# Performance work log

Measured on AMD Instinct MI355X. Metric: run time of the kernel, lower is better.

## Reference

```python
import jax, jax.numpy as jnp
import numpy as np

B, T, C, H = 8, 2048, 512, 512


def setup_inputs() -> dict:
    key = jax.random.key(0)
    ks = jax.random.split(key, 9)
    s = 1.0 / np.sqrt(C)
    return {
        "q": jax.random.normal(ks[0], (B, T, C), jnp.float32),
        "k": jax.random.normal(ks[1], (B, T, C), jnp.float32),
        "v": jax.random.normal(ks[2], (B, T, C), jnp.float32),
        "Wq": jax.random.normal(ks[3], (C, H), jnp.float32) * s,
        "bq": jax.random.normal(ks[4], (H,), jnp.float32) * 0.01,
        "Wk": jax.random.normal(ks[5], (C, H), jnp.float32) * s,
        "bk": jax.random.normal(ks[6], (H,), jnp.float32) * 0.01,
        "Wv": jax.random.normal(ks[7], (C, H), jnp.float32) * s,
        "bv": jax.random.normal(ks[8], (H,), jnp.float32) * 0.01,
    }


def reference(q, k, v, Wq, bq, Wk, bk, Wv, bv):
    # Linear projections (Real_Linear == nn.Linear): [B,T,C] @ [C,H] + [H]
    query = jnp.einsum('btc,ch->bth', q, Wq) + bq
    key_p = jnp.einsum('btc,ch->bth', k, Wk) + bk
    value = jnp.einsum('btc,ch->bth', v, Wv) + bv
    # energy = Q @ K^T / sqrt(H)  -> [B, T, T]
    energy = jnp.einsum('bth,byh->bty', query, key_p) / jnp.sqrt(jnp.asarray(H, query.dtype))
    attn = jax.nn.softmax(energy, axis=-1)
    # weighted value: [B, T, T] @ [B, T, H] -> [B, T, H]
    return jnp.einsum('bty,byh->bth', attn, value)
```

## Files before the change

kernel.cpp:

```cpp
#include <hip/hip_runtime.h>
#include <hip/hip_bf16.h>

typedef unsigned short u16;
typedef unsigned int u32;
typedef short s16x8 __attribute__((ext_vector_type(8)));
typedef float f32x4 __attribute__((ext_vector_type(4)));

#define NB 8
#define NT 2048
#define NC 512
#define NH 512

__device__ __forceinline__ u16 f2bf(float f) {
  unsigned u = __float_as_uint(f);
  u += 0x7FFFu + ((u >> 16) & 1u);
  return (u16)(u >> 16);
}

__device__ __forceinline__ void gld16(const u16* src, u16* lds_dst) {
  __builtin_amdgcn_global_load_lds(
      (const __attribute__((address_space(1))) u32*)src,
      (__attribute__((address_space(3))) u32*)lds_dst, 16, 0, 0);
}

__global__ __launch_bounds__(256) void wt_kernel(const float* __restrict__ W,
                                                 u16* __restrict__ WT) {
  __shared__ float tile[32][33];
  const int x = threadIdx.x & 31;
  const int y = threadIdx.x >> 5;
  const int k0 = blockIdx.x * 32, h0 = blockIdx.y * 32;
#pragma unroll
  for (int p = 0; p < 4; ++p)
    tile[y + 8 * p][x] = W[(size_t)(k0 + y + 8 * p) * NH + h0 + x];
  __syncthreads();
#pragma unroll
  for (int p = 0; p < 4; ++p)
    WT[(size_t)(h0 + y + 8 * p) * NC + k0 + x] = f2bf(tile[x][y + 8 * p]);
}

__global__ __launch_bounds__(256) void proj_kernel(const float* __restrict__ X,
                                                   const u16* __restrict__ WT,
                                                   const float* __restrict__ bias,
                                                   u16* __restrict__ Y) {
  __shared__ __align__(16) u16 Asub[2][128 * 40];
  __shared__ __align__(16) u16 Bsub[2][128 * 40];
  const int t = threadIdx.x;
  const int lane = t & 63;
  const int w = t >> 6;
  const int l16 = lane & 15;
  const int ko8 = (lane >> 4) * 8;
  const int m0 = blockIdx.y * 128;
  const int n0 = blockIdx.x * 128;
  const int wr = (w >> 1) * 64, wc = (w & 1) * 64;
  f32x4 acc[4][4] = {};

  float4 areg[4];
  int4 breg[2];
#define PLOAD(kt)                                                              \
  {                                                                            \
    const int k0_ = (kt) * 32;                                                 \
    _Pragma("unroll")                                                          \
    for (int p = 0; p < 4; ++p) {                                              \
      int c = t + 256 * p;                                                     \
      areg[p] = *(const float4*)&X[(size_t)(m0 + (c >> 3)) * NC + k0_ + (c & 7) * 4]; \
    }                                                                          \
    _Pragma("unroll")                                                          \
    for (int p = 0; p < 2; ++p) {                                              \
      int c = t + 256 * p;                                                     \
      breg[p] = *(const int4*)&WT[(size_t)(n0 + (c >> 2)) * NC + k0_ + (c & 3) * 8];  \
    }                                                                          \
  }
#define PWRITE(buf)                                                            \
  {                                                                            \
    _Pragma("unroll")                                                          \
    for (int p = 0; p < 4; ++p) {                                              \
      int c = t + 256 * p;                                                     \
      ushort4 bb;                                                              \
      bb.x = f2bf(areg[p].x); bb.y = f2bf(areg[p].y);                          \
      bb.z = f2bf(areg[p].z); bb.w = f2bf(areg[p].w);                          \
      *(ushort4*)&Asub[buf][(c >> 3) * 40 + (c & 7) * 4] = bb;                 \
    }                                                                          \
    _Pragma("unroll")                                                          \
    for (int p = 0; p < 2; ++p) {                                              \
      int c = t + 256 * p;                                                     \
      *(int4*)&Bsub[buf][(c >> 2) * 40 + (c & 3) * 8] = breg[p];               \
    }                                                                          \
  }

  PLOAD(0)
  PWRITE(0)
  __syncthreads();

  int pb = 0;
  for (int kt = 0; kt < 16; ++kt) {
    if (kt < 15) PLOAD(kt + 1)
    s16x8 af[4], bf[4];
#pragma unroll
    for (int i = 0; i < 4; ++i)
      af[i] = *(const s16x8*)&Asub[pb][(wr + i * 16 + l16) * 40 + ko8];
#pragma unroll
    for (int j = 0; j < 4; ++j)
      bf[j] = *(const s16x8*)&Bsub[pb][(wc + j * 16 + l16) * 40 + ko8];
#pragma unroll
    for (int i = 0; i < 4; ++i)
#pragma unroll
      for (int j = 0; j < 4; ++j)
        acc[i][j] = __builtin_amdgcn_mfma_f32_16x16x32_bf16(af[i], bf[j], acc[i][j], 0, 0, 0);
    if (kt < 15) PWRITE(pb ^ 1)
    __syncthreads();
    pb ^= 1;
  }
#undef PLOAD
#undef PWRITE
  const int rg = (lane >> 4) * 4;
#pragma unroll
  for (int i = 0; i < 4; ++i)
#pragma unroll
    for (int j = 0; j < 4; ++j) {
      const int col = n0 + wc + j * 16 + l16;
      const float bcol = bias[col];
#pragma unroll
      for (int jj = 0; jj < 4; ++jj) {
        const int row = m0 + wr + i * 16 + rg + jj;
        Y[(size_t)row * NH + col] = f2bf(acc[i][j][jj] + bcol);
      }
    }
}

__global__ __launch_bounds__(256) void vt_kernel(const u16* __restrict__ Vp,
                                                 u16* __restrict__ VpT) {
  __shared__ u16 tile[32][33];
  const int x = threadIdx.x & 31;
  const int y = threadIdx.x >> 5;
  const int t0 = blockIdx.x * 32, h0 = blockIdx.y * 32, b = blockIdx.z;
  const u16* src = Vp + (size_t)b * NT * NH;
  u16* dst = VpT + (size_t)b * NH * NT;
#pragma unroll
  for (int p = 0; p < 4; ++p)
    tile[y + 8 * p][x] = src[(size_t)(t0 + y + 8 * p) * NH + h0 + x];
  __syncthreads();
#pragma unroll
  for (int p = 0; p < 4; ++p)
    dst[(size_t)(h0 + y + 8 * p) * NT + t0 + x] = tile[x][y + 8 * p];
}

__global__ __launch_bounds__(512, 2) void flash_partial(const u16* __restrict__ Qp,
                                                        const u16* __restrict__ Kp,
                                                        const u16* __restrict__ VpT,
                                                        float* __restrict__ O0,
                                                        float* __restrict__ O1,
                                                        float* __restrict__ mlws) {
  __shared__ __align__(16) u16 Klds[2][32 * 512];
  __shared__ __align__(16) u16 Vlds[2][32 * 512];

  const int t = threadIdx.x;
  const int lane = t & 63;
  const int w = t >> 6;
  const int l16 = lane & 15;
  const int g = lane >> 4;
  const int g8 = g * 8;
  const int b = blockIdx.x;
  const int q0 = blockIdx.y * 128;
  const int z = blockIdx.z;
  const int qg = q0 + w * 16 + l16;
  const float kscale = 0.044194173824159216f;

  s16x8 qf[16];
  {
    const u16* qrow = Qp + (size_t)(b * NT + qg) * NH;
#pragma unroll
    for (int ks = 0; ks < 16; ++ks)
      qf[ks] = *(const s16x8*)&qrow[ks * 32 + g8];
  }

  f32x4 oacc[32] = {};
  float m_run = -1e30f, l_run = 0.f;

  const u16* kbat = Kp + (size_t)(b * NT + z * 1024) * NH;
  const u16* vbat = VpT + (size_t)b * NH * NT + z * 1024;

#define STAGE(buf, it)                                                         \
  {                                                                            \
    _Pragma("unroll")                                                          \
    for (int r = 0; r < 4; ++r) {                                              \
      const int i = w * 4 + r;                                      \
      gld16(kbat + (size_t)((it) * 32 + ((i & 1) << 4) + l16) * NH             \
                 + ((i >> 1) << 5) + g8,                                       \
            &Klds[buf][i * 512]);                                              \
      gld16(vbat + (size_t)(i * 16 + l16) * NT + (it) * 32 + g8,               \
            &Vlds[buf][i * 512]);                                              \
    }                                                                          \
  }

  STAGE(0, 0)
  __syncthreads();

  int pb = 0;
  for (int it = 0; it < 32; ++it) {
    if (it < 31) STAGE(pb ^ 1, it + 1)
    f32x4 s0 = {}, s1 = {};
    __builtin_amdgcn_s_setprio(1);
#pragma unroll
    for (int ks = 0; ks < 16; ++ks) {
      s16x8 kf0 = *(const s16x8*)&Klds[pb][(ks * 2 + 0) * 512 + lane * 8];
      s16x8 kf1 = *(const s16x8*)&Klds[pb][(ks * 2 + 1) * 512 + lane * 8];
      s0 = __builtin_amdgcn_mfma_f32_16x16x32_bf16(kf0, qf[ks], s0, 0, 0, 0);
      s1 = __builtin_amdgcn_mfma_f32_16x16x32_bf16(kf1, qf[ks], s1, 0, 0, 0);
    }
    __builtin_amdgcn_s_setprio(0);
    float pv[8];
#pragma unroll
    for (int j = 0; j < 4; ++j) { pv[j] = s0[j] * kscale; pv[4 + j] = s1[j] * kscale; }
    float mx = pv[0];
#pragma unroll
    for (int j = 1; j < 8; ++j) mx = fmaxf(mx, pv[j]);
    mx = fmaxf(mx, __shfl_xor(mx, 16, 64));
    mx = fmaxf(mx, __shfl_xor(mx, 32, 64));
    if (__any(mx > m_run + 8.f)) {
      const float m_new = fmaxf(m_run, mx);
      const float scale = __expf(m_run - m_new);
#pragma unroll
      for (int ht = 0; ht < 32; ++ht) {
        oacc[ht][0] *= scale; oacc[ht][1] *= scale;
        oacc[ht][2] *= scale; oacc[ht][3] *= scale;
      }
      l_run *= scale;
      m_run = m_new;
    }
    float ts = 0.f;
#pragma unroll
    for (int j = 0; j < 8; ++j) { pv[j] = __expf(pv[j] - m_run); ts += pv[j]; }
    ts += __shfl_xor(ts, 16, 64);
    ts += __shfl_xor(ts, 32, 64);
    l_run += ts;
    u32 b0 = ((u32)f2bf(pv[1]) << 16) | f2bf(pv[0]);
    u32 b1 = ((u32)f2bf(pv[3]) << 16) | f2bf(pv[2]);
    u32 b2 = ((u32)f2bf(pv[5]) << 16) | f2bf(pv[4]);
    u32 b3 = ((u32)f2bf(pv[7]) << 16) | f2bf(pv[6]);
    const int srcA = (g & 1) * 32 + l16;
    const int srcB = srcA + 16;
    u32 x0 = (u32)__shfl((int)b0, srcA, 64);
    u32 x1 = (u32)__shfl((int)b1, srcA, 64);
    u32 x2 = (u32)__shfl((int)b2, srcA, 64);
    u32 x3 = (u32)__shfl((int)b3, srcA, 64);
    u32 y0 = (u32)__shfl((int)b0, srcB, 64);
    u32 y1 = (u32)__shfl((int)b1, srcB, 64);
    u32 y2 = (u32)__shfl((int)b2, srcB, 64);
    u32 y3 = (u32)__shfl((int)b3, srcB, 64);
    const bool hi = (lane >> 5) & 1;
    union { u32 u[4]; s16x8 v; } pf;
    pf.u[0] = hi ? x2 : x0;
    pf.u[1] = hi ? x3 : x1;
    pf.u[2] = hi ? y2 : y0;
    pf.u[3] = hi ? y3 : y1;
    __builtin_amdgcn_s_setprio(1);
#pragma unroll
    for (int ht = 0; ht < 32; ++ht) {
      s16x8 vf = *(const s16x8*)&Vlds[pb][ht * 512 + lane * 8];
      oacc[ht] = __builtin_amdgcn_mfma_f32_16x16x32_bf16(vf, pf.v, oacc[ht], 0, 0, 0);
    }
    __builtin_amdgcn_s_setprio(0);
    __syncthreads();
    pb ^= 1;
  }
  float* obase = (z ? O1 : O0) + (size_t)(b * NT + qg) * NH;
#pragma unroll
  for (int ht = 0; ht < 32; ++ht) {
    float4 st;
    st.x = oacc[ht][0]; st.y = oacc[ht][1];
    st.z = oacc[ht][2]; st.w = oacc[ht][3];
    *(float4*)&obase[ht * 16 + g * 4] = st;
  }
  if (g == 0) {
    const size_t row = (size_t)b * NT + qg;
    mlws[row * 4 + z * 2 + 0] = m_run;
    mlws[row * 4 + z * 2 + 1] = l_run;
  }
#undef STAGE
}

__global__ __launch_bounds__(128) void merge_kernel(float* __restrict__ out,
                                                    const float* __restrict__ O1,
                                                    const float* __restrict__ mlws) {
  const size_t row = blockIdx.x;
  const float m0 = mlws[row * 4 + 0], l0 = mlws[row * 4 + 1];
  const float m1 = mlws[row * 4 + 2], l1 = mlws[row * 4 + 3];
  const float m = fmaxf(m0, m1);
  const float a0 = __expf(m0 - m), a1 = __expf(m1 - m);
  const float inv = 1.f / (a0 * l0 + a1 * l1);
  const float c0 = a0 * inv, c1 = a1 * inv;
  const size_t idx = row * NH + threadIdx.x * 4;
  float4 o0 = *(const float4*)&out[idx];
  float4 o1 = *(const float4*)&O1[idx];
  float4 r;
  r.x = c0 * o0.x + c1 * o1.x;
  r.y = c0 * o0.y + c1 * o1.y;
  r.z = c0 * o0.z + c1 * o1.z;
  r.w = c0 * o0.w + c1 * o1.w;
  *(float4*)&out[idx] = r;
}

__global__ __launch_bounds__(256, 1) void flash_kernel(const u16* __restrict__ Qp,
                                                       const u16* __restrict__ Kp,
                                                       const u16* __restrict__ VpT,
                                                       float* __restrict__ out) {
  __shared__ __align__(16) u16 Klds[2][32 * 512];
  __shared__ __align__(16) u16 Vlds[2][32 * 512];

  const int t = threadIdx.x;
  const int lane = t & 63;
  const int w = t >> 6;
  const int l16 = lane & 15;
  const int g = lane >> 4;
  const int g8 = g * 8;
  const int b = blockIdx.x;
  const int q0 = blockIdx.y * 64;
  const int qg = q0 + w * 16 + l16;
  const float kscale = 0.044194173824159216f;

  s16x8 qf[16];
  {
    const u16* qrow = Qp + (size_t)(b * NT + qg) * NH;
#pragma unroll
    for (int ks = 0; ks < 16; ++ks)
      qf[ks] = *(const s16x8*)&qrow[ks * 32 + g8];
  }
  f32x4 oacc[32] = {};
  float m_run = -1e30f, l_run = 0.f;
  const u16* kbat = Kp + (size_t)b * NT * NH;
  const u16* vbat = VpT + (size_t)b * NH * NT;

#pragma unroll
  for (int r = 0; r < 8; ++r) {
    const int i = w * 8 + r;
    gld16(kbat + (size_t)(((i & 1) << 4) + l16) * NH + ((i >> 1) << 5) + g8,
          &Klds[0][i * 512]);
    gld16(vbat + (size_t)(i * 16 + l16) * NT + g8, &Vlds[0][i * 512]);
  }
  __syncthreads();

  int pb = 0;
  for (int it = 0; it < 64; ++it) {
    if (it < 63) {
      const int kv1 = (it + 1) * 32;
      const int nb = pb ^ 1;
#pragma unroll
      for (int r = 0; r < 8; ++r) {
        const int i = w * 8 + r;
        gld16(kbat + (size_t)(kv1 + ((i & 1) << 4) + l16) * NH + ((i >> 1) << 5) + g8,
              &Klds[nb][i * 512]);
        gld16(vbat + (size_t)(i * 16 + l16) * NT + kv1 + g8, &Vlds[nb][i * 512]);
      }
    }
    f32x4 s0 = {}, s1 = {};
#pragma unroll
    for (int ks = 0; ks < 16; ++ks) {
      s16x8 kf0 = *(const s16x8*)&Klds[pb][(ks * 2 + 0) * 512 + lane * 8];
      s16x8 kf1 = *(const s16x8*)&Klds[pb][(ks * 2 + 1) * 512 + lane * 8];
      s0 = __builtin_amdgcn_mfma_f32_16x16x32_bf16(kf0, qf[ks], s0, 0, 0, 0);
      s1 = __builtin_amdgcn_mfma_f32_16x16x32_bf16(kf1, qf[ks], s1, 0, 0, 0);
    }
    float pv[8];
#pragma unroll
    for (int j = 0; j < 4; ++j) { pv[j] = s0[j] * kscale; pv[4 + j] = s1[j] * kscale; }
    float mx = pv[0];
#pragma unroll
    for (int j = 1; j < 8; ++j) mx = fmaxf(mx, pv[j]);
    mx = fmaxf(mx, __shfl_xor(mx, 16, 64));
    mx = fmaxf(mx, __shfl_xor(mx, 32, 64));
    if (__any(mx > m_run)) {
      const float m_new = fmaxf(m_run, mx);
      const float scale = __expf(m_run - m_new);
#pragma unroll
      for (int ht = 0; ht < 32; ++ht) {
        oacc[ht][0] *= scale; oacc[ht][1] *= scale;
        oacc[ht][2] *= scale; oacc[ht][3] *= scale;
      }
      l_run *= scale;
      m_run = m_new;
    }
    float ts = 0.f;
#pragma unroll
    for (int j = 0; j < 8; ++j) { pv[j] = __expf(pv[j] - m_run); ts += pv[j]; }
    ts += __shfl_xor(ts, 16, 64);
    ts += __shfl_xor(ts, 32, 64);
    l_run += ts;
    u32 b0 = ((u32)f2bf(pv[1]) << 16) | f2bf(pv[0]);
    u32 b1 = ((u32)f2bf(pv[3]) << 16) | f2bf(pv[2]);
    u32 b2 = ((u32)f2bf(pv[5]) << 16) | f2bf(pv[4]);
    u32 b3 = ((u32)f2bf(pv[7]) << 16) | f2bf(pv[6]);
    const int srcA = (g & 1) * 32 + l16;
    const int srcB = srcA + 16;
    u32 x0 = (u32)__shfl((int)b0, srcA, 64);
    u32 x1 = (u32)__shfl((int)b1, srcA, 64);
    u32 x2 = (u32)__shfl((int)b2, srcA, 64);
    u32 x3 = (u32)__shfl((int)b3, srcA, 64);
    u32 y0 = (u32)__shfl((int)b0, srcB, 64);
    u32 y1 = (u32)__shfl((int)b1, srcB, 64);
    u32 y2 = (u32)__shfl((int)b2, srcB, 64);
    u32 y3 = (u32)__shfl((int)b3, srcB, 64);
    const bool hi = (lane >> 5) & 1;
    union { u32 u[4]; s16x8 v; } pf;
    pf.u[0] = hi ? x2 : x0;
    pf.u[1] = hi ? x3 : x1;
    pf.u[2] = hi ? y2 : y0;
    pf.u[3] = hi ? y3 : y1;
#pragma unroll
    for (int ht = 0; ht < 32; ++ht) {
      s16x8 vf = *(const s16x8*)&Vlds[pb][ht * 512 + lane * 8];
      oacc[ht] = __builtin_amdgcn_mfma_f32_16x16x32_bf16(vf, pf.v, oacc[ht], 0, 0, 0);
    }
    __syncthreads();
    pb ^= 1;
  }
  const float inv = 1.f / l_run;
  float* obase = out + (size_t)(b * NT + qg) * NH;
#pragma unroll
  for (int ht = 0; ht < 32; ++ht) {
    float4 st;
    st.x = oacc[ht][0] * inv; st.y = oacc[ht][1] * inv;
    st.z = oacc[ht][2] * inv; st.w = oacc[ht][3] * inv;
    *(float4*)&obase[ht * 16 + g * 4] = st;
  }
}

extern "C" void kernel_launch(void* const* d_in, const int* in_sizes, int n_in,
                              void* d_out, int out_size, void* d_ws, size_t ws_size,
                              hipStream_t stream) {
  (void)in_sizes; (void)n_in; (void)out_size;
  const float* q  = (const float*)d_in[0];
  const float* k  = (const float*)d_in[1];
  const float* v  = (const float*)d_in[2];
  const float* Wq = (const float*)d_in[3];
  const float* bq = (const float*)d_in[4];
  const float* Wk = (const float*)d_in[5];
  const float* bk = (const float*)d_in[6];
  const float* Wv = (const float*)d_in[7];
  const float* bv = (const float*)d_in[8];
  float* out = (float*)d_out;

  u16* ws   = (u16*)d_ws;
  u16* WqT  = ws;
  u16* WkT  = WqT + (size_t)NC * NH;
  u16* WvT  = WkT + (size_t)NC * NH;
  u16* Qp   = WvT + (size_t)NC * NH;
  u16* Kp   = Qp + (size_t)NB * NT * NH;
  u16* Vp   = Kp + (size_t)NB * NT * NH;
  u16* VpT  = Vp + (size_t)NB * NT * NH;
  u16* endb = VpT + (size_t)NB * NT * NH;
  float* O1   = (float*)endb;
  float* mlws = O1 + (size_t)NB * NT * NH;
  const size_t need = (size_t)((char*)(mlws + (size_t)NB * NT * 4) - (char*)d_ws);

  wt_kernel<<<dim3(16, 16), 256, 0, stream>>>(Wq, WqT);
  wt_kernel<<<dim3(16, 16), 256, 0, stream>>>(Wk, WkT);
  wt_kernel<<<dim3(16, 16), 256, 0, stream>>>(Wv, WvT);

  proj_kernel<<<dim3(4, 128), 256, 0, stream>>>(q, WqT, bq, Qp);
  proj_kernel<<<dim3(4, 128), 256, 0, stream>>>(k, WkT, bk, Kp);
  proj_kernel<<<dim3(4, 128), 256, 0, stream>>>(v, WvT, bv, Vp);

  vt_kernel<<<dim3(64, 16, NB), 256, 0, stream>>>(Vp, VpT);

  if (ws_size >= need) {
    flash_partial<<<dim3(NB, NT / 128, 2), 512, 0, stream>>>(Qp, Kp, VpT, out, O1, mlws);
    merge_kernel<<<dim3(NB * NT), 128, 0, stream>>>(out, O1, mlws);
  } else {
    flash_kernel<<<dim3(NB, NT / 64), 256, 0, stream>>>(Qp, Kp, VpT, out);
  }
}
```

Baseline: 228.6 us.

## Permute V^T layout to drop P shuffles; batch projection and weight-transpose launches

The V transpose kernel now stores keys in a permuted column order. The P·V product can then use the probabilities each lane already holds, split into two 16x16x16 bf16 MFMAs, instead of eight cross-lane shuffles and selects per tile. The per-lane row-sum reduction moves out of the loop to the end. The three weight-transpose and three projection launches are merged into single launches using blockIdx.z. The fallback kernel also picks up the lazy rescale threshold. The trade is twice as many, smaller MFMA instructions in the P·V loop.

```diff
diff --git a/kernel.cpp b/kernel.cpp
--- a/kernel.cpp
+++ b/kernel.cpp
@@ -4,6 +4,7 @@
 typedef unsigned short u16;
 typedef unsigned int u32;
 typedef short s16x8 __attribute__((ext_vector_type(8)));
+typedef short s16x4 __attribute__((ext_vector_type(4)));
 typedef float f32x4 __attribute__((ext_vector_type(4)));
 
 #define NB 8
@@ -11,6 +12,12 @@
 #define NC 512
 #define NH 512
 
+#if __has_builtin(__builtin_amdgcn_mfma_f32_16x16x16_bf16)
+#define MFMA_PV(va, pb, c) __builtin_amdgcn_mfma_f32_16x16x16_bf16(va, pb, c, 0, 0, 0)
+#else
+#define MFMA_PV(va, pb, c) __builtin_amdgcn_mfma_f32_16x16x16bf16_1k(va, pb, c, 0, 0, 0)
+#endif
+
 __device__ __forceinline__ u16 f2bf(float f) {
   unsigned u = __float_as_uint(f);
   u += 0x7FFFu + ((u >> 16) & 1u);
@@ -23,9 +30,15 @@
       (__attribute__((address_space(3))) u32*)lds_dst, 16, 0, 0);
 }
 
-__global__ __launch_bounds__(256) void wt_kernel(const float* __restrict__ W,
-                                                 u16* __restrict__ WT) {
+__global__ __launch_bounds__(256) void wt_kernel(const float* __restrict__ Wq,
+                                                 const float* __restrict__ Wk,
+                                                 const float* __restrict__ Wv,
+                                                 u16* __restrict__ WqT,
+                                                 u16* __restrict__ WkT,
+                                                 u16* __restrict__ WvT) {
   __shared__ float tile[32][33];
+  const float* W = (blockIdx.z == 0) ? Wq : (blockIdx.z == 1) ? Wk : Wv;
+  u16* WT = (blockIdx.z == 0) ? WqT : (blockIdx.z == 1) ? WkT : WvT;
   const int x = threadIdx.x & 31;
   const int y = threadIdx.x >> 5;
   const int k0 = blockIdx.x * 32, h0 = blockIdx.y * 32;
@@ -38,12 +51,26 @@
     WT[(size_t)(h0 + y + 8 * p) * NC + k0 + x] = f2bf(tile[x][y + 8 * p]);
 }
 
-__global__ __launch_bounds__(256) void proj_kernel(const float* __restrict__ X,
-                                                   const u16* __restrict__ WT,
-                                                   const float* __restrict__ bias,
-                                                   u16* __restrict__ Y) {
+__global__ __launch_bounds__(256) void proj_kernel(const float* __restrict__ Xq,
+                                                   const float* __restrict__ Xk,
+                                                   const float* __restrict__ Xv,
+                                                   const u16* __restrict__ WqT,
+                                                   const u16* __restrict__ WkT,
+                                                   const u16* __restrict__ WvT,
+                                                   const float* __restrict__ bq,
+                                                   const float* __restrict__ bk,
+                                                   const float* __restrict__ bv,
+                                                   u16* __restrict__ Yq,
+                                                   u16* __restrict__ Yk,
+                                                   u16* __restrict__ Yv) {
   __shared__ __align__(16) u16 Asub[2][128 * 40];
   __shared__ __align__(16) u16 Bsub[2][128 * 40];
+  const int zz = blockIdx.z;
+  const float* X = (zz == 0) ? Xq : (zz == 1) ? Xk : Xv;
+  const u16* WT = (zz == 0) ? WqT : (zz == 1) ? WkT : WvT;
+  const float* bias = (zz == 0) ? bq : (zz == 1) ? bk : bv;
+  u16* Y = (zz == 0) ? Yq : (zz == 1) ? Yk : Yv;
+
   const int t = threadIdx.x;
   const int lane = t & 63;
   const int w = t >> 6;
@@ -135,13 +162,14 @@
   const int t0 = blockIdx.x * 32, h0 = blockIdx.y * 32, b = blockIdx.z;
   const u16* src = Vp + (size_t)b * NT * NH;
   u16* dst = VpT + (size_t)b * NH * NT;
+  const int xp = ((x & 15) >> 2) * 8 + (x >> 4) * 4 + (x & 3);
 #pragma unroll
   for (int p = 0; p < 4; ++p)
     tile[y + 8 * p][x] = src[(size_t)(t0 + y + 8 * p) * NH + h0 + x];
   __syncthreads();
 #pragma unroll
   for (int p = 0; p < 4; ++p)
-    dst[(size_t)(h0 + y + 8 * p) * NT + t0 + x] = tile[x][y + 8 * p];
+    dst[(size_t)(h0 + y + 8 * p) * NT + t0 + xp] = tile[x][y + 8 * p];
 }
 
 __global__ __launch_bounds__(512, 2) void flash_partial(const u16* __restrict__ Qp,
@@ -230,34 +258,20 @@
     float ts = 0.f;
 #pragma unroll
     for (int j = 0; j < 8; ++j) { pv[j] = __expf(pv[j] - m_run); ts += pv[j]; }
-    ts += __shfl_xor(ts, 16, 64);
-    ts += __shfl_xor(ts, 32, 64);
     l_run += ts;
-    u32 b0 = ((u32)f2bf(pv[1]) << 16) | f2bf(pv[0]);
-    u32 b1 = ((u32)f2bf(pv[3]) << 16) | f2bf(pv[2]);
-    u32 b2 = ((u32)f2bf(pv[5]) << 16) | f2bf(pv[4]);
-    u32 b3 = ((u32)f2bf(pv[7]) << 16) | f2bf(pv[6]);
-    const int srcA = (g & 1) * 32 + l16;
-    const int srcB = srcA + 16;
-    u32 x0 = (u32)__shfl((int)b0, srcA, 64);
-    u32 x1 = (u32)__shfl((int)b1, srcA, 64);
-    u32 x2 = (u32)__shfl((int)b2, srcA, 64);
-    u32 x3 = (u32)__shfl((int)b3, srcA, 64);
-    u32 y0 = (u32)__shfl((int)b0, srcB, 64);
-    u32 y1 = (u32)__shfl((int)b1, srcB, 64);
-    u32 y2 = (u32)__shfl((int)b2, srcB, 64);
-    u32 y3 = (u32)__shfl((int)b3, srcB, 64);
-    const bool hi = (lane >> 5) & 1;
-    union { u32 u[4]; s16x8 v; } pf;
-    pf.u[0] = hi ? x2 : x0;
-    pf.u[1] = hi ? x3 : x1;
-    pf.u[2] = hi ? y2 : y0;
-    pf.u[3] = hi ? y3 : y1;
+    union { u32 u[2]; s16x4 v; } plo, phi;
+    plo.u[0] = ((u32)f2bf(pv[1]) << 16) | f2bf(pv[0]);
+    plo.u[1] = ((u32)f2bf(pv[3]) << 16) | f2bf(pv[2]);
+    phi.u[0] = ((u32)f2bf(pv[5]) << 16) | f2bf(pv[4]);
+    phi.u[1] = ((u32)f2bf(pv[7]) << 16) | f2bf(pv[6]);
     __builtin_amdgcn_s_setprio(1);
 #pragma unroll
     for (int ht = 0; ht < 32; ++ht) {
       s16x8 vf = *(const s16x8*)&Vlds[pb][ht * 512 + lane * 8];
-      oacc[ht] = __builtin_amdgcn_mfma_f32_16x16x32_bf16(vf, pf.v, oacc[ht], 0, 0, 0);
+      s16x4 vlo = __builtin_shufflevector(vf, vf, 0, 1, 2, 3);
+      s16x4 vhi = __builtin_shufflevector(vf, vf, 4, 5, 6, 7);
+      oacc[ht] = MFMA_PV(vlo, plo.v, oacc[ht]);
+      oacc[ht] = MFMA_PV(vhi, phi.v, oacc[ht]);
     }
     __builtin_amdgcn_s_setprio(0);
     __syncthreads();
@@ -271,10 +285,13 @@
     st.z = oacc[ht][2]; st.w = oacc[ht][3];
     *(float4*)&obase[ht * 16 + g * 4] = st;
   }
+  float lt = l_run;
+  lt += __shfl_xor(lt, 16, 64);
+  lt += __shfl_xor(lt, 32, 64);
   if (g == 0) {
     const size_t row = (size_t)b * NT + qg;
     mlws[row * 4 + z * 2 + 0] = m_run;
-    mlws[row * 4 + z * 2 + 1] = l_run;
+    mlws[row * 4 + z * 2 + 1] = lt;
   }
 #undef STAGE
 }
@@ -368,7 +385,7 @@
     for (int j = 1; j < 8; ++j) mx = fmaxf(mx, pv[j]);
     mx = fmaxf(mx, __shfl_xor(mx, 16, 64));
     mx = fmaxf(mx, __shfl_xor(mx, 32, 64));
-    if (__any(mx > m_run)) {
+    if (__any(mx > m_run + 8.f)) {
       const float m_new = fmaxf(m_run, mx);
       const float scale = __expf(m_run - m_new);
 #pragma unroll
@@ -382,38 +399,27 @@
     float ts = 0.f;
 #pragma unroll
     for (int j = 0; j < 8; ++j) { pv[j] = __expf(pv[j] - m_run); ts += pv[j]; }
-    ts += __shfl_xor(ts, 16, 64);
-    ts += __shfl_xor(ts, 32, 64);
     l_run += ts;
-    u32 b0 = ((u32)f2bf(pv[1]) << 16) | f2bf(pv[0]);
-    u32 b1 = ((u32)f2bf(pv[3]) << 16) | f2bf(pv[2]);
-    u32 b2 = ((u32)f2bf(pv[5]) << 16) | f2bf(pv[4]);
-    u32 b3 = ((u32)f2bf(pv[7]) << 16) | f2bf(pv[6]);
-    const int srcA = (g & 1) * 32 + l16;
-    const int srcB = srcA + 16;
-    u32 x0 = (u32)__shfl((int)b0, srcA, 64);
-    u32 x1 = (u32)__shfl((int)b1, srcA, 64);
-    u32 x2 = (u32)__shfl((int)b2, srcA, 64);
-    u32 x3 = (u32)__shfl((int)b3, srcA, 64);
-    u32 y0 = (u32)__shfl((int)b0, srcB, 64);
-    u32 y1 = (u32)__shfl((int)b1, srcB, 64);
-    u32 y2 = (u32)__shfl((int)b2, srcB, 64);
-    u32 y3 = (u32)__shfl((int)b3, srcB, 64);
-    const bool hi = (lane >> 5) & 1;
-    union { u32 u[4]; s16x8 v; } pf;
-    pf.u[0] = hi ? x2 : x0;
-    pf.u[1] = hi ? x3 : x1;
-    pf.u[2] = hi ? y2 : y0;
-    pf.u[3] = hi ? y3 : y1;
+    union { u32 u[2]; s16x4 v; } plo, phi;
+    plo.u[0] = ((u32)f2bf(pv[1]) << 16) | f2bf(pv[0]);
+    plo.u[1] = ((u32)f2bf(pv[3]) << 16) | f2bf(pv[2]);
+    phi.u[0] = ((u32)f2bf(pv[5]) << 16) | f2bf(pv[4]);
+    phi.u[1] = ((u32)f2bf(pv[7]) << 16) | f2bf(pv[6]);
 #pragma unroll
     for (int ht = 0; ht < 32; ++ht) {
       s16x8 vf = *(const s16x8*)&Vlds[pb][ht * 512 + lane * 8];
-      oacc[ht] = __builtin_amdgcn_mfma_f32_16x16x32_bf16(vf, pf.v, oacc[ht], 0, 0, 0);
+      s16x4 vlo = __builtin_shufflevector(vf, vf, 0, 1, 2, 3);
+      s16x4 vhi = __builtin_shufflevector(vf, vf, 4, 5, 6, 7);
+      oacc[ht] = MFMA_PV(vlo, plo.v, oacc[ht]);
+      oacc[ht] = MFMA_PV(vhi, phi.v, oacc[ht]);
     }
     __syncthreads();
     pb ^= 1;
   }
-  const float inv = 1.f / l_run;
+  float lt = l_run;
+  lt += __shfl_xor(lt, 16, 64);
+  lt += __shfl_xor(lt, 32, 64);
+  const float inv = 1.f / lt;
   float* obase = out + (size_t)(b * NT + qg) * NH;
 #pragma unroll
   for (int ht = 0; ht < 32; ++ht) {
@@ -452,13 +458,10 @@
   float* mlws = O1 + (size_t)NB * NT * NH;
   const size_t need = (size_t)((char*)(mlws + (size_t)NB * NT * 4) - (char*)d_ws);
 
-  wt_kernel<<<dim3(16, 16), 256, 0, stream>>>(Wq, WqT);
-  wt_kernel<<<dim3(16, 16), 256, 0, stream>>>(Wk, WkT);
-  wt_kernel<<<dim3(16, 16), 256, 0, stream>>>(Wv, WvT);
-
-  proj_kernel<<<dim3(4, 128), 256, 0, stream>>>(q, WqT, bq, Qp);
-  proj_kernel<<<dim3(4, 128), 256, 0, stream>>>(k, WkT, bk, Kp);
-  proj_kernel<<<dim3(4, 128), 256, 0, stream>>>(v, WvT, bv, Vp);
+  wt_kernel<<<dim3(16, 16, 3), 256, 0, stream>>>(Wq, Wk, Wv, WqT, WkT, WvT);
+
+  proj_kernel<<<dim3(4, 128, 3), 256, 0, stream>>>(q, k, v, WqT, WkT, WvT,
+                                                   bq, bk, bv, Qp, Kp, Vp);
 
   vt_kernel<<<dim3(64, 16, NB), 256, 0, stream>>>(Vp, VpT);
 
```

Result: no change. 232.8 us (+1.8%).
